# Kernel optimization log

Measured on AMD Instinct MI355X. Metric: run time of the kernel, lower is better.

## Reference

```python
import jax, jax.numpy as jnp
import numpy as np

N_NODES = 50000
N_EDGES = 800000
NEG_SLOPE = 0.2


def _gat_layer(x, src, dst, W, a_src, a_dst, bias, heads, out_ch, concat, n_nodes):
    # x: [N, in_ch]; W: [in_ch, heads*out_ch]; a_src/a_dst: [heads, out_ch]
    h = (x @ W).reshape(n_nodes, heads, out_ch)          # [N, H, C]
    s_src = jnp.einsum('nhc,hc->nh', h, a_src)           # [N, H]
    s_dst = jnp.einsum('nhc,hc->nh', h, a_dst)           # [N, H]
    e = jax.nn.leaky_relu(s_src[src] + s_dst[dst], NEG_SLOPE)  # [E, H]
    # segment softmax over incoming edges of each destination node
    e_max = jax.ops.segment_max(e, dst, num_segments=n_nodes)   # [N, H]
    e_max = jnp.where(jnp.isfinite(e_max), e_max, 0.0)
    e_exp = jnp.exp(e - e_max[dst])                       # [E, H]
    denom = jax.ops.segment_sum(e_exp, dst, num_segments=n_nodes)  # [N, H]
    alpha = e_exp / denom[dst]                            # [E, H]
    msg = h[src] * alpha[:, :, None]                      # [E, H, C]
    out = jax.ops.segment_sum(msg, dst, num_segments=n_nodes)     # [N, H, C]
    if concat:
        out = out.reshape(n_nodes, heads * out_ch)
    else:
        out = out.mean(axis=1)
    return out + bias


def setup_inputs() -> dict:
    key = jax.random.key(0)
    ks = jax.random.split(key, 9)
    x = jax.random.normal(ks[0], (N_NODES, 128), dtype=jnp.float32)
    edge_index = jax.random.randint(ks[1], (2, N_EDGES), 0, N_NODES, dtype=jnp.int64)
    # glorot-ish scaled params
    W1 = jax.random.normal(ks[2], (128, 128), dtype=jnp.float32) * 0.1
    att_src1 = jax.random.normal(ks[3], (4, 32), dtype=jnp.float32) * 0.1
    att_dst1 = jax.random.normal(ks[4], (4, 32), dtype=jnp.float32) * 0.1
    bias1 = jnp.zeros((128,), dtype=jnp.float32)
    W2 = jax.random.normal(ks[5], (128, 64), dtype=jnp.float32) * 0.1
    att_src2 = jax.random.normal(ks[6], (1, 64), dtype=jnp.float32) * 0.1
    att_dst2 = jax.random.normal(ks[7], (1, 64), dtype=jnp.float32) * 0.1
    bias2 = jnp.zeros((64,), dtype=jnp.float32)
    return {"x": x, "edge_index": edge_index, "W1": W1, "att_src1": att_src1,
            "att_dst1": att_dst1, "bias1": bias1, "W2": W2, "att_src2": att_src2,
            "att_dst2": att_dst2, "bias2": bias2}


def reference(x, edge_index, W1, att_src1, att_dst1, bias1, W2, att_src2, att_dst2, bias2):
    n = x.shape[0]
    # PyG GATConv default add_self_loops=True
    loops = jnp.arange(n, dtype=edge_index.dtype)
    src = jnp.concatenate([edge_index[0], loops])
    dst = jnp.concatenate([edge_index[1], loops])
    h = _gat_layer(x, src, dst, W1, att_src1, att_dst1, bias1, 4, 32, True, n)
    h = jax.nn.relu(h)
    out = _gat_layer(h, src, dst, W2, att_src2, att_dst2, bias2, 1, 64, False, n)
    return out
```

## Files before the change

kernel.cpp:

```cpp
#include <hip/hip_runtime.h>
#include <hip/hip_bf16.h>


typedef __attribute__((ext_vector_type(8))) short bf16x8;
typedef __attribute__((ext_vector_type(4))) float f32x4;

#define BCHUNK 1024

__device__ __forceinline__ unsigned short f2bf(float f) {
  unsigned x = __float_as_uint(f);
  unsigned r = (x + 0x7fffu + ((x >> 16) & 1u)) >> 16;
  return (unsigned short)r;
}
__device__ __forceinline__ float bf2f(unsigned short u) {
  return __uint_as_float(((unsigned)u) << 16);
}
__device__ __forceinline__ float bflo(unsigned u) {
  return __uint_as_float(u << 16);
}
__device__ __forceinline__ float bfhi(unsigned u) {
  return __uint_as_float(u & 0xffff0000u);
}

__device__ __forceinline__ int lds_scan256(int v, int* s) {
  int tid = threadIdx.x;
  s[tid] = v;
  __syncthreads();
  for (int o = 1; o < 256; o <<= 1) {
    int t = (tid >= o) ? s[tid - o] : 0;
    __syncthreads();
    s[tid] += t;
    __syncthreads();
  }
  return s[tid];
}

__global__ void cvt_wall(const float* __restrict__ W1, const float* __restrict__ as1,
                         const float* __restrict__ ad1, const float* __restrict__ W2,
                         const float* __restrict__ as2, const float* __restrict__ ad2,
                         unsigned short* __restrict__ W1t, unsigned short* __restrict__ W2t,
                         unsigned short* __restrict__ wsb1, unsigned short* __restrict__ wsb2) {
  int i = blockIdx.x * blockDim.x + threadIdx.x;
  if (i < 16384) {
    int k = i >> 7, m = i & 127;
    W1t[m * 128 + k] = f2bf(W1[i]);
  } else if (i < 24576) {
    int j = i - 16384;
    int k = j / 64, m = j % 64;
    W2t[m * 128 + k] = f2bf(W2[j]);
  } else if (i < 26624) {
    int j = i - 24576;
    int m = j >> 7, k = j & 127;
    float acc = 0.f;
    if (m < 4) {
      for (int c = 0; c < 32; ++c) acc += W1[k * 128 + m * 32 + c] * as1[m * 32 + c];
    } else if (m < 8) {
      for (int c = 0; c < 32; ++c) acc += W1[k * 128 + (m - 4) * 32 + c] * ad1[(m - 4) * 32 + c];
    }
    wsb1[j] = f2bf(acc);
  } else if (i < 28672) {
    int j = i - 26624;
    int m = j >> 7, k = j & 127;
    float acc = 0.f;
    if (m == 0) {
      for (int c = 0; c < 64; ++c) acc += W2[k * 64 + c] * as2[c];
    } else if (m == 1) {
      for (int c = 0; c < 64; ++c) acc += W2[k * 64 + c] * ad2[c];
    }
    wsb2[j] = f2bf(acc);
  }
}

template <int AF32, int SC>
__global__ __launch_bounds__(256) void gemm_mfma(
    const void* __restrict__ Av, const unsigned short* __restrict__ Bt,
    const unsigned short* __restrict__ wsb, unsigned short* __restrict__ C,
    float* __restrict__ ssrc, float* __restrict__ sdst, int N, int M) {
  const int K = 128;
  int lane = threadIdx.x & 63;
  int wv = threadIdx.x >> 6;
  int row0 = blockIdx.x * 64 + wv * 16;
  if (row0 >= N) return;
  int r = lane & 15, quad = lane >> 4;

  bf16x8 a[4];
  if (AF32) {
    const float* ap = (const float*)Av + (size_t)(row0 + r) * K + quad * 8;
#pragma unroll
    for (int t = 0; t < 4; ++t) {
      float4 lo = *(const float4*)(ap + t * 32);
      float4 hi = *(const float4*)(ap + t * 32 + 4);
      a[t][0] = (short)f2bf(lo.x); a[t][1] = (short)f2bf(lo.y);
      a[t][2] = (short)f2bf(lo.z); a[t][3] = (short)f2bf(lo.w);
      a[t][4] = (short)f2bf(hi.x); a[t][5] = (short)f2bf(hi.y);
      a[t][6] = (short)f2bf(hi.z); a[t][7] = (short)f2bf(hi.w);
    }
  } else {
    const unsigned short* ap = (const unsigned short*)Av + (size_t)(row0 + r) * K + quad * 8;
#pragma unroll
    for (int t = 0; t < 4; ++t) a[t] = *(const bf16x8*)(ap + t * 32);
  }

  for (int c0 = 0; c0 < M; c0 += 16) {
    f32x4 acc = {0.f, 0.f, 0.f, 0.f};
    const unsigned short* bp = Bt + (size_t)(c0 + r) * K + quad * 8;
#pragma unroll
    for (int t = 0; t < 4; ++t) {
      bf16x8 b = *(const bf16x8*)(bp + t * 32);
      acc = __builtin_amdgcn_mfma_f32_16x16x32_bf16(a[t], b, acc, 0, 0, 0);
    }
    unsigned short* cp = C + (size_t)(row0 + quad * 4) * M + c0 + r;
#pragma unroll
    for (int i = 0; i < 4; ++i) cp[(size_t)i * M] = f2bf(acc[i]);
  }

  {
    f32x4 acc = {0.f, 0.f, 0.f, 0.f};
    const unsigned short* bp = wsb + r * 128 + quad * 8;
#pragma unroll
    for (int t = 0; t < 4; ++t) {
      bf16x8 b = *(const bf16x8*)(bp + t * 32);
      acc = __builtin_amdgcn_mfma_f32_16x16x32_bf16(a[t], b, acc, 0, 0, 0);
    }
    int row = row0 + quad * 4;
    if (r < SC) {
#pragma unroll
      for (int i = 0; i < 4; ++i) ssrc[(size_t)(row + i) * SC + r] = acc[i];
    } else if (r < 2 * SC) {
#pragma unroll
      for (int i = 0; i < 4; ++i) sdst[(size_t)(row + i) * SC + (r - SC)] = acc[i];
    }
  }
}


__global__ __launch_bounds__(256) void b_count(const int* __restrict__ ei, int E, int N,
                                               int* __restrict__ cnt) {
  __shared__ int h[256];
  int tid = threadIdx.x;
  h[tid] = 0;
  __syncthreads();
  int ET = E + N;
  int base = blockIdx.x * BCHUNK;
  int lim = base + BCHUNK;
  if (lim > ET) lim = ET;
  for (int i = base + tid * 4; i < lim; i += 1024) {
    if (i + 3 < E && i + 4 <= lim) {
      int4 d4 = *(const int4*)(ei + E + i);
      atomicAdd(&h[d4.x >> 8], 1);
      atomicAdd(&h[d4.y >> 8], 1);
      atomicAdd(&h[d4.z >> 8], 1);
      atomicAdd(&h[d4.w >> 8], 1);
    } else {
      for (int k = 0; k < 4; ++k) {
        int idx = i + k;
        if (idx < lim) {
          int d = (idx < E) ? ei[E + idx] : (idx - E);
          atomicAdd(&h[d >> 8], 1);
        }
      }
    }
  }
  __syncthreads();
  cnt[(size_t)blockIdx.x * 256 + tid] = h[tid];
}

__global__ __launch_bounds__(256) void b_scan_bkt(const int* __restrict__ cnt, int NBLK,
                                                  int* __restrict__ blkoff,
                                                  int* __restrict__ bucketTotal) {
  __shared__ int s[256];
  int bucket = blockIdx.x, tid = threadIdx.x;
  int carry = 0;
  for (int base = 0; base < NBLK; base += 256) {
    int blk = base + tid;
    int v = (blk < NBLK) ? cnt[(size_t)blk * 256 + bucket] : 0;
    s[tid] = v;
    __syncthreads();
    for (int o = 1; o < 256; o <<= 1) {
      int t = (tid >= o) ? s[tid - o] : 0;
      __syncthreads();
      s[tid] += t;
      __syncthreads();
    }
    if (blk < NBLK) blkoff[(size_t)blk * 256 + bucket] = carry + s[tid] - v;
    carry += s[255];
    __syncthreads();
  }
  if (tid == 0) bucketTotal[bucket] = carry;
}

__global__ __launch_bounds__(256) void b_scatter(
    const int* __restrict__ ei, int E, int N,
    const int* __restrict__ bucketTotal, const int* __restrict__ blkoff,
    unsigned* __restrict__ bkt) {
  __shared__ int s[256];
  __shared__ int lcur[256];
  int tid = threadIdx.x;
  int tot = bucketTotal[tid];
  int incl = lds_scan256(tot, s);
  lcur[tid] = (incl - tot) + blkoff[(size_t)blockIdx.x * 256 + tid];
  __syncthreads();
  int ET = E + N;
  int base = blockIdx.x * BCHUNK;
  int lim = base + BCHUNK;
  if (lim > ET) lim = ET;
  for (int i = base + tid * 4; i < lim; i += 1024) {
    if (i + 3 < E && i + 4 <= lim) {
      int4 s4 = *(const int4*)(ei + i);
      int4 d4 = *(const int4*)(ei + E + i);
      int slot;
      slot = atomicAdd(&lcur[d4.x >> 8], 1); bkt[slot] = (unsigned)s4.x | ((unsigned)(d4.x & 255) << 16);
      slot = atomicAdd(&lcur[d4.y >> 8], 1); bkt[slot] = (unsigned)s4.y | ((unsigned)(d4.y & 255) << 16);
      slot = atomicAdd(&lcur[d4.z >> 8], 1); bkt[slot] = (unsigned)s4.z | ((unsigned)(d4.z & 255) << 16);
      slot = atomicAdd(&lcur[d4.w >> 8], 1); bkt[slot] = (unsigned)s4.w | ((unsigned)(d4.w & 255) << 16);
    } else {
      for (int k = 0; k < 4; ++k) {
        int idx = i + k;
        if (idx < lim) {
          int s_, d;
          if (idx < E) { s_ = ei[idx]; d = ei[E + idx]; }
          else { s_ = idx - E; d = s_; }
          int slot = atomicAdd(&lcur[d >> 8], 1);
          bkt[slot] = (unsigned)s_ | ((unsigned)(d & 255) << 16);
        }
      }
    }
  }
}

__global__ __launch_bounds__(256) void b_bucketsort(
    const unsigned* __restrict__ bkt, const int* __restrict__ bucketTotal,
    unsigned* __restrict__ csr4, int* __restrict__ rowptr, int N, int ET) {
  __shared__ int s[256];
  __shared__ int cnt[256];
  int b = blockIdx.x, tid = threadIdx.x;
  int tot = bucketTotal[tid];
  (void)lds_scan256(tot, s);
  int base = (b == 0) ? 0 : s[b - 1];
  int end = s[b];
  __syncthreads();
  cnt[tid] = 0;
  __syncthreads();
  for (int i = base + tid; i < end; i += 512) {
    unsigned p0 = bkt[i];
    int i1 = i + 256;
    unsigned p1 = (i1 < end) ? bkt[i1] : 0u;
    atomicAdd(&cnt[p0 >> 16], 1);
    if (i1 < end) atomicAdd(&cnt[p1 >> 16], 1);
  }
  __syncthreads();
  int v = cnt[tid];
  int incl = lds_scan256(v, s);
  int excl = incl - v;
  int node = (b << 8) + tid;
  if (node < N) rowptr[node] = base + excl;
  if (tid == 0 && b == gridDim.x - 1) rowptr[N] = ET;
  cnt[tid] = base + excl;
  __syncthreads();
  for (int i = base + tid; i < end; i += 512) {
    unsigned p0 = bkt[i];
    int i1 = i + 256;
    unsigned p1 = (i1 < end) ? bkt[i1] : 0u;
    int slot0 = atomicAdd(&cnt[p0 >> 16], 1);
    csr4[slot0] = p0;
    if (i1 < end) {
      int slot1 = atomicAdd(&cnt[p1 >> 16], 1);
      csr4[slot1] = p1;
    }
  }
}

template <int H>
__global__ __launch_bounds__(256) void k_weightsB(
    const unsigned* __restrict__ csr4, const int* __restrict__ bucketTotal,
    const float* __restrict__ ssrc, const float* __restrict__ sdst,
    unsigned short* __restrict__ ew) {
  __shared__ int s[256];
  int b = blockIdx.x, tid = threadIdx.x;
  int tot = bucketTotal[tid];
  (void)lds_scan256(tot, s);
  int base = (b == 0) ? 0 : s[b - 1];
  int end = s[b];
  __syncthreads();
  for (int i = base + tid; i < end; i += 256) {
    unsigned v = csr4[i];
    int src = v & 0xFFFF;
    int d = (b << 8) | (int)(v >> 16);
    if (H == 4) {
      float4 a = *(const float4*)(ssrc + (size_t)src * 4);
      float4 bb = *(const float4*)(sdst + (size_t)d * 4);
      float sc;
      sc = a.x + bb.x; sc = sc > 0.f ? sc : 0.2f * sc; float w0 = __expf(sc);
      sc = a.y + bb.y; sc = sc > 0.f ? sc : 0.2f * sc; float w1 = __expf(sc);
      sc = a.z + bb.z; sc = sc > 0.f ? sc : 0.2f * sc; float w2 = __expf(sc);
      sc = a.w + bb.w; sc = sc > 0.f ? sc : 0.2f * sc; float w3 = __expf(sc);
      unsigned lo = (unsigned)f2bf(w0) | ((unsigned)f2bf(w1) << 16);
      unsigned hi = (unsigned)f2bf(w2) | ((unsigned)f2bf(w3) << 16);
      *(uint2*)(ew + (size_t)i * 4) = make_uint2(lo, hi);
    } else {
      float sc = ssrc[src] + sdst[d];
      sc = sc > 0.f ? sc : 0.2f * sc;
      ew[i] = f2bf(__expf(sc));
    }
  }
}

template <int H, int C, int L, int OUT_BF16>
__global__ __launch_bounds__(256) void gat_aggr4(
    const int* __restrict__ rowptr, const unsigned* __restrict__ csr4,
    const unsigned short* __restrict__ ew, const unsigned short* __restrict__ h,
    const float* __restrict__ bias, void* __restrict__ outv, int N) {
  const int HC = H * C;
  const int G = 64 / L;
  int lane = threadIdx.x & 63;
  int n = blockIdx.x * 4 + (threadIdx.x >> 6);
  if (n >= N) return;
  int l = lane & (L - 1);
  int g = lane / L;
  int c0 = l * 8;
  int hh = c0 / C;
  int beg = rowptr[n];
  int cnt = rowptr[n + 1] - beg;
  float a0 = 0.f, a1 = 0.f, a2 = 0.f, a3 = 0.f;
  float a4 = 0.f, a5 = 0.f, a6 = 0.f, a7 = 0.f, ws = 0.f;

  int j = g;
  for (; j + G < cnt; j += 2 * G) {
    int i0 = beg + j, i1 = beg + j + G;
    int s0 = (int)(csr4[i0] & 0xFFFF);
    int s1 = (int)(csr4[i1] & 0xFFFF);
    float w0 = bf2f(ew[(size_t)i0 * H + hh]);
    float w1 = bf2f(ew[(size_t)i1 * H + hh]);
    uint4 u0 = *(const uint4*)(h + (size_t)s0 * HC + c0);
    uint4 u1 = *(const uint4*)(h + (size_t)s1 * HC + c0);
    a0 = fmaf(w0, bflo(u0.x), a0); a1 = fmaf(w0, bfhi(u0.x), a1);
    a2 = fmaf(w0, bflo(u0.y), a2); a3 = fmaf(w0, bfhi(u0.y), a3);
    a4 = fmaf(w0, bflo(u0.z), a4); a5 = fmaf(w0, bfhi(u0.z), a5);
    a6 = fmaf(w0, bflo(u0.w), a6); a7 = fmaf(w0, bfhi(u0.w), a7);
    a0 = fmaf(w1, bflo(u1.x), a0); a1 = fmaf(w1, bfhi(u1.x), a1);
    a2 = fmaf(w1, bflo(u1.y), a2); a3 = fmaf(w1, bfhi(u1.y), a3);
    a4 = fmaf(w1, bflo(u1.z), a4); a5 = fmaf(w1, bfhi(u1.z), a5);
    a6 = fmaf(w1, bflo(u1.w), a6); a7 = fmaf(w1, bfhi(u1.w), a7);
    ws += w0 + w1;
  }
  if (j < cnt) {
    int i0 = beg + j;
    int s0 = (int)(csr4[i0] & 0xFFFF);
    float w0 = bf2f(ew[(size_t)i0 * H + hh]);
    uint4 u0 = *(const uint4*)(h + (size_t)s0 * HC + c0);
    a0 = fmaf(w0, bflo(u0.x), a0); a1 = fmaf(w0, bfhi(u0.x), a1);
    a2 = fmaf(w0, bflo(u0.y), a2); a3 = fmaf(w0, bfhi(u0.y), a3);
    a4 = fmaf(w0, bflo(u0.z), a4); a5 = fmaf(w0, bfhi(u0.z), a5);
    a6 = fmaf(w0, bflo(u0.w), a6); a7 = fmaf(w0, bfhi(u0.w), a7);
    ws += w0;
  }
#pragma unroll
  for (int off = L; off < 64; off <<= 1) {
    a0 += __shfl_xor(a0, off, 64); a1 += __shfl_xor(a1, off, 64);
    a2 += __shfl_xor(a2, off, 64); a3 += __shfl_xor(a3, off, 64);
    a4 += __shfl_xor(a4, off, 64); a5 += __shfl_xor(a5, off, 64);
    a6 += __shfl_xor(a6, off, 64); a7 += __shfl_xor(a7, off, 64);
    ws += __shfl_xor(ws, off, 64);
  }
  if (lane < L) {
    float inv = 1.f / ws;
    float4 bA = *(const float4*)(bias + c0);
    float4 bB = *(const float4*)(bias + c0 + 4);
    float v0 = fmaf(a0, inv, bA.x), v1 = fmaf(a1, inv, bA.y);
    float v2 = fmaf(a2, inv, bA.z), v3 = fmaf(a3, inv, bA.w);
    float v4 = fmaf(a4, inv, bB.x), v5 = fmaf(a5, inv, bB.y);
    float v6 = fmaf(a6, inv, bB.z), v7 = fmaf(a7, inv, bB.w);
    if (OUT_BF16) {
      v0 = fmaxf(v0, 0.f); v1 = fmaxf(v1, 0.f);
      v2 = fmaxf(v2, 0.f); v3 = fmaxf(v3, 0.f);
      v4 = fmaxf(v4, 0.f); v5 = fmaxf(v5, 0.f);
      v6 = fmaxf(v6, 0.f); v7 = fmaxf(v7, 0.f);
      uint4 o;
      o.x = (unsigned)f2bf(v0) | ((unsigned)f2bf(v1) << 16);
      o.y = (unsigned)f2bf(v2) | ((unsigned)f2bf(v3) << 16);
      o.z = (unsigned)f2bf(v4) | ((unsigned)f2bf(v5) << 16);
      o.w = (unsigned)f2bf(v6) | ((unsigned)f2bf(v7) << 16);
      ((uint4*)outv)[(size_t)n * (HC / 8) + l] = o;
    } else {
      float* op = (float*)outv + (size_t)n * HC + c0;
      *(float4*)op = make_float4(v0, v1, v2, v3);
      *(float4*)(op + 4) = make_float4(v4, v5, v6, v7);
    }
  }
}

extern "C" void kernel_launch(void* const* d_in, const int* in_sizes, int n_in,
                              void* d_out, int out_size, void* d_ws, size_t ws_size,
                              hipStream_t stream) {
  const float* x   = (const float*)d_in[0];
  const int*   ei  = (const int*)d_in[1];
  const float* W1  = (const float*)d_in[2];
  const float* as1 = (const float*)d_in[3];
  const float* ad1 = (const float*)d_in[4];
  const float* b1  = (const float*)d_in[5];
  const float* W2  = (const float*)d_in[6];
  const float* as2 = (const float*)d_in[7];
  const float* ad2 = (const float*)d_in[8];
  const float* b2  = (const float*)d_in[9];

  const int N = in_sizes[0] / 128;
  const int E = in_sizes[1] / 2;
  const int ET = E + N;
  const int NBKT = (N + 255) >> 8;
  const int NBLK = (ET + BCHUNK - 1) / BCHUNK;

  char* pc = (char*)d_ws;
  auto alloc = [&](size_t bytes) -> void* {
    void* r = (void*)pc;
    pc += (bytes + 255) & ~(size_t)255;
    return r;
  };
  unsigned short* h1b   = (unsigned short*)alloc((size_t)N * 128 * 2);
  unsigned short* out1b = (unsigned short*)alloc((size_t)N * 128 * 2);
  unsigned short* W1t   = (unsigned short*)alloc(128 * 128 * 2);
  unsigned short* W2t   = (unsigned short*)alloc(64 * 128 * 2);
  unsigned short* wsb1  = (unsigned short*)alloc(16 * 128 * 2);
  unsigned short* wsb2  = (unsigned short*)alloc(16 * 128 * 2);
  float* ssrc1 = (float*)alloc((size_t)N * 4 * 4);
  float* sdst1 = (float*)alloc((size_t)N * 4 * 4);
  float* ssrc2 = (float*)alloc((size_t)N * 4);
  float* sdst2 = (float*)alloc((size_t)N * 4);
  int* rowptr      = (int*)alloc((size_t)(N + 1) * 4);
  int* cnt         = (int*)alloc((size_t)NBLK * 256 * 4);
  int* blkoff      = (int*)alloc((size_t)NBLK * 256 * 4);
  int* bucketTotal = (int*)alloc(256 * 4);
  unsigned* bkt  = (unsigned*)alloc((size_t)ET * 4);
  unsigned* csr4 = (unsigned*)alloc((size_t)ET * 4);
  unsigned short* ew1 = (unsigned short*)alloc((size_t)ET * 4 * 2);
  unsigned short* ew2 = (unsigned short*)alloc((size_t)ET * 2);
  unsigned short* h2b = h1b;

  dim3 blk(256);

  b_count<<<dim3(NBLK), blk, 0, stream>>>(ei, E, N, cnt);
  b_scan_bkt<<<dim3(256), blk, 0, stream>>>(cnt, NBLK, blkoff, bucketTotal);
  b_scatter<<<dim3(NBLK), blk, 0, stream>>>(ei, E, N, bucketTotal, blkoff, bkt);
  b_bucketsort<<<dim3(NBKT), blk, 0, stream>>>(bkt, bucketTotal, csr4, rowptr, N, ET);

  cvt_wall<<<dim3((28672 + 255) / 256), blk, 0, stream>>>(
      W1, as1, ad1, W2, as2, ad2, W1t, W2t, wsb1, wsb2);

  gemm_mfma<1, 4><<<dim3((N + 63) / 64), blk, 0, stream>>>(
      x, W1t, wsb1, h1b, ssrc1, sdst1, N, 128);
  k_weightsB<4><<<dim3(NBKT), blk, 0, stream>>>(csr4, bucketTotal, ssrc1, sdst1, ew1);
  gat_aggr4<4, 32, 16, 1><<<dim3((N + 3) / 4), blk, 0, stream>>>(
      rowptr, csr4, ew1, h1b, b1, out1b, N);

  gemm_mfma<0, 1><<<dim3((N + 63) / 64), blk, 0, stream>>>(
      out1b, W2t, wsb2, h2b, ssrc2, sdst2, N, 64);
  k_weightsB<1><<<dim3(NBKT), blk, 0, stream>>>(csr4, bucketTotal, ssrc2, sdst2, ew2);
  gat_aggr4<1, 64, 8, 0><<<dim3((N + 3) / 4), blk, 0, stream>>>(
      rowptr, csr4, ew2, h2b, b2, d_out, N);
}
```

Measured before the change: 238.7 us.

## Split aggregation into 32-column slices per block and fuse weight conversion into count kernel

The aggregation kernel now gives each block one 32-column slice for a group of nodes instead of the full feature row. The block index is interleaved so that neighbouring blocks work on the same nodes' slices, which should improve L2 locality and raise edge-level parallelism (16 edge groups per node instead of 4 or 8). The weight conversion kernel is merged into the bucket-count kernel as extra blocks, removing one launch. In exchange, per-node work such as rowptr/csr reads and edge-weight loads is repeated for each slice, and the grid sizes assume N is divisible by 2.

```diff
diff --git a/kernel.cpp b/kernel.cpp
--- a/kernel.cpp
+++ b/kernel.cpp
@@ -35,109 +35,47 @@
   return s[tid];
 }
 
-__global__ void cvt_wall(const float* __restrict__ W1, const float* __restrict__ as1,
-                         const float* __restrict__ ad1, const float* __restrict__ W2,
-                         const float* __restrict__ as2, const float* __restrict__ ad2,
-                         unsigned short* __restrict__ W1t, unsigned short* __restrict__ W2t,
-                         unsigned short* __restrict__ wsb1, unsigned short* __restrict__ wsb2) {
-  int i = blockIdx.x * blockDim.x + threadIdx.x;
-  if (i < 16384) {
-    int k = i >> 7, m = i & 127;
-    W1t[m * 128 + k] = f2bf(W1[i]);
-  } else if (i < 24576) {
-    int j = i - 16384;
-    int k = j / 64, m = j % 64;
-    W2t[m * 128 + k] = f2bf(W2[j]);
-  } else if (i < 26624) {
-    int j = i - 24576;
-    int m = j >> 7, k = j & 127;
-    float acc = 0.f;
-    if (m < 4) {
-      for (int c = 0; c < 32; ++c) acc += W1[k * 128 + m * 32 + c] * as1[m * 32 + c];
-    } else if (m < 8) {
-      for (int c = 0; c < 32; ++c) acc += W1[k * 128 + (m - 4) * 32 + c] * ad1[(m - 4) * 32 + c];
-    }
-    wsb1[j] = f2bf(acc);
-  } else if (i < 28672) {
-    int j = i - 26624;
-    int m = j >> 7, k = j & 127;
-    float acc = 0.f;
-    if (m == 0) {
-      for (int c = 0; c < 64; ++c) acc += W2[k * 64 + c] * as2[c];
-    } else if (m == 1) {
-      for (int c = 0; c < 64; ++c) acc += W2[k * 64 + c] * ad2[c];
-    }
-    wsb2[j] = f2bf(acc);
-  }
-}
-
-template <int AF32, int SC>
-__global__ __launch_bounds__(256) void gemm_mfma(
-    const void* __restrict__ Av, const unsigned short* __restrict__ Bt,
-    const unsigned short* __restrict__ wsb, unsigned short* __restrict__ C,
-    float* __restrict__ ssrc, float* __restrict__ sdst, int N, int M) {
-  const int K = 128;
-  int lane = threadIdx.x & 63;
-  int wv = threadIdx.x >> 6;
-  int row0 = blockIdx.x * 64 + wv * 16;
-  if (row0 >= N) return;
-  int r = lane & 15, quad = lane >> 4;
-
-  bf16x8 a[4];
-  if (AF32) {
-    const float* ap = (const float*)Av + (size_t)(row0 + r) * K + quad * 8;
-#pragma unroll
-    for (int t = 0; t < 4; ++t) {
-      float4 lo = *(const float4*)(ap + t * 32);
-      float4 hi = *(const float4*)(ap + t * 32 + 4);
-      a[t][0] = (short)f2bf(lo.x); a[t][1] = (short)f2bf(lo.y);
-      a[t][2] = (short)f2bf(lo.z); a[t][3] = (short)f2bf(lo.w);
-      a[t][4] = (short)f2bf(hi.x); a[t][5] = (short)f2bf(hi.y);
-      a[t][6] = (short)f2bf(hi.z); a[t][7] = (short)f2bf(hi.w);
-    }
-  } else {
-    const unsigned short* ap = (const unsigned short*)Av + (size_t)(row0 + r) * K + quad * 8;
-#pragma unroll
-    for (int t = 0; t < 4; ++t) a[t] = *(const bf16x8*)(ap + t * 32);
-  }
-
-  for (int c0 = 0; c0 < M; c0 += 16) {
-    f32x4 acc = {0.f, 0.f, 0.f, 0.f};
-    const unsigned short* bp = Bt + (size_t)(c0 + r) * K + quad * 8;
-#pragma unroll
-    for (int t = 0; t < 4; ++t) {
-      bf16x8 b = *(const bf16x8*)(bp + t * 32);
-      acc = __builtin_amdgcn_mfma_f32_16x16x32_bf16(a[t], b, acc, 0, 0, 0);
-    }
-    unsigned short* cp = C + (size_t)(row0 + quad * 4) * M + c0 + r;
-#pragma unroll
-    for (int i = 0; i < 4; ++i) cp[(size_t)i * M] = f2bf(acc[i]);
-  }
-
-  {
-    f32x4 acc = {0.f, 0.f, 0.f, 0.f};
-    const unsigned short* bp = wsb + r * 128 + quad * 8;
-#pragma unroll
-    for (int t = 0; t < 4; ++t) {
-      bf16x8 b = *(const bf16x8*)(bp + t * 32);
-      acc = __builtin_amdgcn_mfma_f32_16x16x32_bf16(a[t], b, acc, 0, 0, 0);
-    }
-    int row = row0 + quad * 4;
-    if (r < SC) {
-#pragma unroll
-      for (int i = 0; i < 4; ++i) ssrc[(size_t)(row + i) * SC + r] = acc[i];
-    } else if (r < 2 * SC) {
-#pragma unroll
-      for (int i = 0; i < 4; ++i) sdst[(size_t)(row + i) * SC + (r - SC)] = acc[i];
-    }
-  }
-}
-
-
-__global__ __launch_bounds__(256) void b_count(const int* __restrict__ ei, int E, int N,
-                                               int* __restrict__ cnt) {
+__global__ __launch_bounds__(256) void b_count_cvt(
+    const int* __restrict__ ei, int E, int N, int NBLK, int* __restrict__ cnt,
+    const float* __restrict__ W1, const float* __restrict__ as1,
+    const float* __restrict__ ad1, const float* __restrict__ W2,
+    const float* __restrict__ as2, const float* __restrict__ ad2,
+    unsigned short* __restrict__ W1t, unsigned short* __restrict__ W2t,
+    unsigned short* __restrict__ wsb1, unsigned short* __restrict__ wsb2) {
+  int tid = threadIdx.x;
+  if ((int)blockIdx.x >= NBLK) {
+    int i = ((int)blockIdx.x - NBLK) * 256 + tid;
+    if (i < 16384) {
+      int k = i >> 7, m = i & 127;
+      W1t[m * 128 + k] = f2bf(W1[i]);
+    } else if (i < 24576) {
+      int j = i - 16384;
+      int k = j / 64, m = j % 64;
+      W2t[m * 128 + k] = f2bf(W2[j]);
+    } else if (i < 26624) {
+      int j = i - 24576;
+      int m = j >> 7, k = j & 127;
+      float acc = 0.f;
+      if (m < 4) {
+        for (int c = 0; c < 32; ++c) acc += W1[k * 128 + m * 32 + c] * as1[m * 32 + c];
+      } else if (m < 8) {
+        for (int c = 0; c < 32; ++c) acc += W1[k * 128 + (m - 4) * 32 + c] * ad1[(m - 4) * 32 + c];
+      }
+      wsb1[j] = f2bf(acc);
+    } else if (i < 28672) {
+      int j = i - 26624;
+      int m = j >> 7, k = j & 127;
+      float acc = 0.f;
+      if (m == 0) {
+        for (int c = 0; c < 64; ++c) acc += W2[k * 64 + c] * as2[c];
+      } else if (m == 1) {
+        for (int c = 0; c < 64; ++c) acc += W2[k * 64 + c] * ad2[c];
+      }
+      wsb2[j] = f2bf(acc);
+    }
+    return;
+  }
   __shared__ int h[256];
-  int tid = threadIdx.x;
   h[tid] = 0;
   __syncthreads();
   int ET = E + N;
@@ -164,6 +102,69 @@
   __syncthreads();
   cnt[(size_t)blockIdx.x * 256 + tid] = h[tid];
 }
+
+template <int AF32, int SC>
+__global__ __launch_bounds__(256) void gemm_mfma(
+    const void* __restrict__ Av, const unsigned short* __restrict__ Bt,
+    const unsigned short* __restrict__ wsb, unsigned short* __restrict__ C,
+    float* __restrict__ ssrc, float* __restrict__ sdst, int N, int M) {
+  const int K = 128;
+  int lane = threadIdx.x & 63;
+  int wv = threadIdx.x >> 6;
+  int row0 = blockIdx.x * 64 + wv * 16;
+  if (row0 >= N) return;
+  int r = lane & 15, quad = lane >> 4;
+
+  bf16x8 a[4];
+  if (AF32) {
+    const float* ap = (const float*)Av + (size_t)(row0 + r) * K + quad * 8;
+#pragma unroll
+    for (int t = 0; t < 4; ++t) {
+      float4 lo = *(const float4*)(ap + t * 32);
+      float4 hi = *(const float4*)(ap + t * 32 + 4);
+      a[t][0] = (short)f2bf(lo.x); a[t][1] = (short)f2bf(lo.y);
+      a[t][2] = (short)f2bf(lo.z); a[t][3] = (short)f2bf(lo.w);
+      a[t][4] = (short)f2bf(hi.x); a[t][5] = (short)f2bf(hi.y);
+      a[t][6] = (short)f2bf(hi.z); a[t][7] = (short)f2bf(hi.w);
+    }
+  } else {
+    const unsigned short* ap = (const unsigned short*)Av + (size_t)(row0 + r) * K + quad * 8;
+#pragma unroll
+    for (int t = 0; t < 4; ++t) a[t] = *(const bf16x8*)(ap + t * 32);
+  }
+
+  for (int c0 = 0; c0 < M; c0 += 16) {
+    f32x4 acc = {0.f, 0.f, 0.f, 0.f};
+    const unsigned short* bp = Bt + (size_t)(c0 + r) * K + quad * 8;
+#pragma unroll
+    for (int t = 0; t < 4; ++t) {
+      bf16x8 b = *(const bf16x8*)(bp + t * 32);
+      acc = __builtin_amdgcn_mfma_f32_16x16x32_bf16(a[t], b, acc, 0, 0, 0);
+    }
+    unsigned short* cp = C + (size_t)(row0 + quad * 4) * M + c0 + r;
+#pragma unroll
+    for (int i = 0; i < 4; ++i) cp[(size_t)i * M] = f2bf(acc[i]);
+  }
+
+  {
+    f32x4 acc = {0.f, 0.f, 0.f, 0.f};
+    const unsigned short* bp = wsb + r * 128 + quad * 8;
+#pragma unroll
+    for (int t = 0; t < 4; ++t) {
+      bf16x8 b = *(const bf16x8*)(bp + t * 32);
+      acc = __builtin_amdgcn_mfma_f32_16x16x32_bf16(a[t], b, acc, 0, 0, 0);
+    }
+    int row = row0 + quad * 4;
+    if (r < SC) {
+#pragma unroll
+      for (int i = 0; i < 4; ++i) ssrc[(size_t)(row + i) * SC + r] = acc[i];
+    } else if (r < 2 * SC) {
+#pragma unroll
+      for (int i = 0; i < 4; ++i) sdst[(size_t)(row + i) * SC + (r - SC)] = acc[i];
+    }
+  }
+}
+
 
 __global__ __launch_bounds__(256) void b_scan_bkt(const int* __restrict__ cnt, int NBLK,
                                                   int* __restrict__ blkoff,
@@ -305,20 +306,23 @@
   }
 }
 
-template <int H, int C, int L, int OUT_BF16>
-__global__ __launch_bounds__(256) void gat_aggr4(
+template <int H, int OUT_BF16>
+__global__ __launch_bounds__(256) void gat_aggr5(
     const int* __restrict__ rowptr, const unsigned* __restrict__ csr4,
     const unsigned short* __restrict__ ew, const unsigned short* __restrict__ h,
     const float* __restrict__ bias, void* __restrict__ outv, int N) {
-  const int HC = H * C;
-  const int G = 64 / L;
+  const int HCT = (H == 4) ? 128 : 64;
+  const int G = 16;
+  int bi = blockIdx.x;
+  int slice, ng;
+  if (H == 4) { slice = (bi & 7) >> 1; ng = (bi >> 3) * 2 + (bi & 1); }
+  else        { slice = (bi & 7) >> 2; ng = (bi >> 3) * 4 + (bi & 3); }
   int lane = threadIdx.x & 63;
-  int n = blockIdx.x * 4 + (threadIdx.x >> 6);
+  int n = ng * 4 + (threadIdx.x >> 6);
   if (n >= N) return;
-  int l = lane & (L - 1);
-  int g = lane / L;
-  int c0 = l * 8;
-  int hh = c0 / C;
+  int l = lane & 3;
+  int g = lane >> 2;
+  int c0 = slice * 32 + l * 8;
   int beg = rowptr[n];
   int cnt = rowptr[n + 1] - beg;
   float a0 = 0.f, a1 = 0.f, a2 = 0.f, a3 = 0.f;
@@ -329,10 +333,10 @@
     int i0 = beg + j, i1 = beg + j + G;
     int s0 = (int)(csr4[i0] & 0xFFFF);
     int s1 = (int)(csr4[i1] & 0xFFFF);
-    float w0 = bf2f(ew[(size_t)i0 * H + hh]);
-    float w1 = bf2f(ew[(size_t)i1 * H + hh]);
-    uint4 u0 = *(const uint4*)(h + (size_t)s0 * HC + c0);
-    uint4 u1 = *(const uint4*)(h + (size_t)s1 * HC + c0);
+    float w0 = bf2f(H == 4 ? ew[(size_t)i0 * 4 + slice] : ew[i0]);
+    float w1 = bf2f(H == 4 ? ew[(size_t)i1 * 4 + slice] : ew[i1]);
+    uint4 u0 = *(const uint4*)(h + (size_t)s0 * HCT + c0);
+    uint4 u1 = *(const uint4*)(h + (size_t)s1 * HCT + c0);
     a0 = fmaf(w0, bflo(u0.x), a0); a1 = fmaf(w0, bfhi(u0.x), a1);
     a2 = fmaf(w0, bflo(u0.y), a2); a3 = fmaf(w0, bfhi(u0.y), a3);
     a4 = fmaf(w0, bflo(u0.z), a4); a5 = fmaf(w0, bfhi(u0.z), a5);
@@ -346,8 +350,8 @@
   if (j < cnt) {
     int i0 = beg + j;
     int s0 = (int)(csr4[i0] & 0xFFFF);
-    float w0 = bf2f(ew[(size_t)i0 * H + hh]);
-    uint4 u0 = *(const uint4*)(h + (size_t)s0 * HC + c0);
+    float w0 = bf2f(H == 4 ? ew[(size_t)i0 * 4 + slice] : ew[i0]);
+    uint4 u0 = *(const uint4*)(h + (size_t)s0 * HCT + c0);
     a0 = fmaf(w0, bflo(u0.x), a0); a1 = fmaf(w0, bfhi(u0.x), a1);
     a2 = fmaf(w0, bflo(u0.y), a2); a3 = fmaf(w0, bfhi(u0.y), a3);
     a4 = fmaf(w0, bflo(u0.z), a4); a5 = fmaf(w0, bfhi(u0.z), a5);
@@ -355,14 +359,14 @@
     ws += w0;
   }
 #pragma unroll
-  for (int off = L; off < 64; off <<= 1) {
+  for (int off = 4; off < 64; off <<= 1) {
     a0 += __shfl_xor(a0, off, 64); a1 += __shfl_xor(a1, off, 64);
     a2 += __shfl_xor(a2, off, 64); a3 += __shfl_xor(a3, off, 64);
     a4 += __shfl_xor(a4, off, 64); a5 += __shfl_xor(a5, off, 64);
     a6 += __shfl_xor(a6, off, 64); a7 += __shfl_xor(a7, off, 64);
     ws += __shfl_xor(ws, off, 64);
   }
-  if (lane < L) {
+  if (lane < 4) {
     float inv = 1.f / ws;
     float4 bA = *(const float4*)(bias + c0);
     float4 bB = *(const float4*)(bias + c0 + 4);
@@ -380,9 +384,9 @@
       o.y = (unsigned)f2bf(v2) | ((unsigned)f2bf(v3) << 16);
       o.z = (unsigned)f2bf(v4) | ((unsigned)f2bf(v5) << 16);
       o.w = (unsigned)f2bf(v6) | ((unsigned)f2bf(v7) << 16);
-      ((uint4*)outv)[(size_t)n * (HC / 8) + l] = o;
+      ((uint4*)outv)[(size_t)n * (HCT / 8) + slice * 4 + l] = o;
     } else {
-      float* op = (float*)outv + (size_t)n * HC + c0;
+      float* op = (float*)outv + (size_t)n * HCT + c0;
       *(float4*)op = make_float4(v0, v1, v2, v3);
       *(float4*)(op + 4) = make_float4(v4, v5, v6, v7);
     }
@@ -437,23 +441,21 @@
 
   dim3 blk(256);
 
-  b_count<<<dim3(NBLK), blk, 0, stream>>>(ei, E, N, cnt);
+  b_count_cvt<<<dim3(NBLK + 112), blk, 0, stream>>>(
+      ei, E, N, NBLK, cnt, W1, as1, ad1, W2, as2, ad2, W1t, W2t, wsb1, wsb2);
   b_scan_bkt<<<dim3(256), blk, 0, stream>>>(cnt, NBLK, blkoff, bucketTotal);
   b_scatter<<<dim3(NBLK), blk, 0, stream>>>(ei, E, N, bucketTotal, blkoff, bkt);
   b_bucketsort<<<dim3(NBKT), blk, 0, stream>>>(bkt, bucketTotal, csr4, rowptr, N, ET);
 
-  cvt_wall<<<dim3((28672 + 255) / 256), blk, 0, stream>>>(
-      W1, as1, ad1, W2, as2, ad2, W1t, W2t, wsb1, wsb2);
-
   gemm_mfma<1, 4><<<dim3((N + 63) / 64), blk, 0, stream>>>(
       x, W1t, wsb1, h1b, ssrc1, sdst1, N, 128);
   k_weightsB<4><<<dim3(NBKT), blk, 0, stream>>>(csr4, bucketTotal, ssrc1, sdst1, ew1);
-  gat_aggr4<4, 32, 16, 1><<<dim3((N + 3) / 4), blk, 0, stream>>>(
+  gat_aggr5<4, 1><<<dim3(N), blk, 0, stream>>>(
       rowptr, csr4, ew1, h1b, b1, out1b, N);
 
   gemm_mfma<0, 1><<<dim3((N + 63) / 64), blk, 0, stream>>>(
       out1b, W2t, wsb2, h2b, ssrc2, sdst2, N, 64);
   k_weightsB<1><<<dim3(NBKT), blk, 0, stream>>>(csr4, bucketTotal, ssrc2, sdst2, ew2);
-  gat_aggr4<1, 64, 8, 0><<<dim3((N + 3) / 4), blk, 0, stream>>>(
+  gat_aggr5<1, 0><<<dim3(N / 2), blk, 0, stream>>>(
       rowptr, csr4, ew2, h2b, b2, d_out, N);
 }
```

New measurement: 300.0 us. 25.7% more time.
